# Optimization experiments

Hardware: AMD Instinct MI355X
Metric: run time of the kernel (lower is better)

## Reference

```python
import jax, jax.numpy as jnp
import numpy as np


def setup_inputs() -> dict:
    B, Lq, Lk, D, F, H = 2, 2048, 2048, 128, 128, 8
    key = jax.random.key(0)
    ks = jax.random.split(key, 8)
    X_Q = jax.random.normal(ks[0], (B, Lq, D), dtype=jnp.float32)
    X_K = jax.random.normal(ks[1], (B, Lk, D), dtype=jnp.float32)
    X_V = jax.random.normal(ks[2], (B, Lk, F), dtype=jnp.float32)
    mask = jax.random.randint(ks[3], (B, 1, Lq, Lk), 0, 2, dtype=jnp.int32)
    # xavier_normal for [H, D, D]: std = sqrt(2/(D+D))
    W_Q = jax.random.normal(ks[4], (H, D, D), dtype=jnp.float32) * np.sqrt(2.0 / (D + D))
    W_K = jax.random.normal(ks[5], (H, D, D), dtype=jnp.float32) * np.sqrt(2.0 / (D + D))
    W_V = jax.random.normal(ks[6], (H, F, F), dtype=jnp.float32) * np.sqrt(2.0 / (F + F))
    O = jax.random.normal(ks[7], (F * H, F), dtype=jnp.float32) * np.sqrt(2.0 / (F * H + F))
    return {"X_Q": X_Q, "X_K": X_K, "X_V": X_V, "mask": mask,
            "W_Q": W_Q, "W_K": W_K, "W_V": W_V, "O": O}


def reference(X_Q, X_K, X_V, mask, W_Q, W_K, W_V, O):
    B, Lq, D = X_Q.shape
    H = W_Q.shape[0]
    F = W_V.shape[1]
    # torch.einsum with repeated in-operand index ('hdd') takes the diagonal
    dq = jnp.diagonal(W_Q, axis1=1, axis2=2)  # [H, D]
    dk = jnp.diagonal(W_K, axis1=1, axis2=2)  # [H, D]
    dv = jnp.diagonal(W_V, axis1=1, axis2=2)  # [H, F]
    g = dq * dk                               # fused per-head QK diagonal scale [H, D]
    scale = 1.0 / jnp.sqrt(jnp.asarray(D, dtype=X_Q.dtype))
    scores = jnp.einsum('bqd,hd,bkd->bhqk', X_Q, g, X_K) * scale  # [B,H,Lq,Lk]
    scores = jnp.where(mask == 0, jnp.asarray(-jnp.inf, scores.dtype), scores)
    A = jax.nn.softmax(scores, axis=-1)
    # O_h = A @ (diag(dv_h) scaled V)
    Oh = jnp.einsum('bhqk,hf,bkf->bhqf', A, dv, X_V)  # [B,H,Lq,F]
    Oh = Oh.transpose(0, 2, 1, 3).reshape(B, Lq, H * F)
    return jnp.einsum('bqx,xf->bqf', Oh, O)
```

## Files before the change

kernel.cpp:

```cpp
#include <hip/hip_runtime.h>

typedef __bf16 bf16;
typedef __bf16 bf16x4 __attribute__((ext_vector_type(4)));
typedef __bf16 bf16x8 __attribute__((ext_vector_type(8)));
typedef float f32x4 __attribute__((ext_vector_type(4)));
typedef unsigned int u32;
typedef unsigned long long u64;

#define B_ 2
#define H_ 8
#define L_ 2048
#define D_ 128
#define F_ 128
#define QT 64
#define KT 64
#define NKT (L_ / KT)

#define WS_KB 0u
#define WS_VT (1u << 20)
#define WS_MB (2u << 20)

#define SMEM_BYTES 75776
#define SP_OFF 65536
#define SP_STRIDE 72
#define LWS_OFF 74752
#define SOH_STRIDE 136
#define SO2_STRIDE 136

__device__ __forceinline__ void dma16(const void* g, void* l) {
    __builtin_amdgcn_global_load_lds(
        (const __attribute__((address_space(1))) u32*)g,
        (__attribute__((address_space(3))) u32*)l, 16, 0, 0);
}

__global__ __launch_bounds__(256)
void prep_all(const float* __restrict__ XK, const float* __restrict__ XV,
              const int* __restrict__ mask, bf16* __restrict__ Kb,
              bf16* __restrict__ Vtb, u64* __restrict__ bits)
{
    const int bid = blockIdx.x;
    const int tid = threadIdx.x;
    if (bid < 8192) {
        int wv = bid * 4 + (tid >> 6);
        int lane = tid & 63;
        size_t base = (size_t)wv * 256;
        #pragma unroll
        for (int s = 0; s < 4; ++s) {
            int m = mask[base + s * 64 + lane];
            u64 bal = __ballot(m != 0);
            if (lane == 0) bits[(size_t)wv * 4 + s] = bal;
        }
    } else if (bid < 8448) {
        int gid = (bid - 8192) * 256 + tid;
        int row = gid >> 4;
        int j   = gid & 15;
        const float* src = XK + (size_t)row * 128 + j * 8;
        float4 v0 = *(const float4*)src;
        float4 v1 = *(const float4*)(src + 4);
        bf16x8 w;
        w[0] = (bf16)v0.x; w[1] = (bf16)v0.y; w[2] = (bf16)v0.z; w[3] = (bf16)v0.w;
        w[4] = (bf16)v1.x; w[5] = (bf16)v1.y; w[6] = (bf16)v1.z; w[7] = (bf16)v1.w;
        int jp = j ^ (row & 15);
        *(bf16x8*)(Kb + (size_t)row * 128 + jp * 8) = w;
    } else {
        int idx  = bid - 8448;
        int tile = idx >> 2;
        int fq   = idx & 3;
        int f    = fq * 32 + (tid & 31);
        int j    = tid >> 5;
        int bb   = tile >> 5, kt = tile & 31;
        const float* src = XV + ((size_t)(bb * L_ + kt * 64 + j * 8)) * F_ + f;
        bf16x8 w;
        #pragma unroll
        for (int jj = 0; jj < 8; ++jj) w[jj] = (bf16)src[(size_t)jj * F_];
        *(bf16x8*)(Vtb + (size_t)tile * 8192 + f * 64 + ((j ^ (f & 7)) * 8)) = w;
    }
}

__global__ __launch_bounds__(256, 2)
void attn_fused_kernel(const float* __restrict__ XQ, const bf16* __restrict__ Kb,
                       const bf16* __restrict__ Vtb, const u64* __restrict__ bits,
                       const float* __restrict__ WQ, const float* __restrict__ WK,
                       const float* __restrict__ WV, const float* __restrict__ Om,
                       float* __restrict__ out)
{
    __shared__ __align__(16) char smem[SMEM_BYTES];
    __shared__ __align__(16) float g_s[128];

    bf16* sK0 = (bf16*)smem;
    bf16* sK1 = (bf16*)(smem + 16384);
    bf16* sV0 = (bf16*)(smem + 32768);
    bf16* sV1 = (bf16*)(smem + 49152);
    bf16* sP  = (bf16*)(smem + SP_OFF);
    float* lws = (float*)(smem + LWS_OFF);
    bf16* sOh  = (bf16*)smem;
    bf16* sO2t = (bf16*)(smem + 17408);

    const int tid  = threadIdx.x;
    const int wave = tid >> 6;
    const int lane = tid & 63;
    const int c    = lane & 15;
    const int quad = lane >> 4;
    const int qt = blockIdx.x, h = blockIdx.y, b = blockIdx.z;
    const int q0 = qt * QT;
    const int mh = wave >> 1;
    const int fh = wave & 1;
    const int fv  = tid & 127;
    const int grp = tid >> 7;

    if (tid < 128) {
        float wq = WQ[(h * D_ + tid) * D_ + tid];
        float wk = WK[(h * D_ + tid) * D_ + tid];
        g_s[tid] = wq * wk * 0.08838834764831845f;
    }
    __syncthreads();

    const char* gKbase = (const char*)Kb + (size_t)(b * L_) * 256;
    const char* gVbase = (const char*)Vtb + (size_t)(b * NKT) * 16384;

    #pragma unroll
    for (int i = 0; i < 4; ++i) dma16(gKbase + i * 4096 + tid * 16, (char*)sK0 + i * 4096 + tid * 16);
    #pragma unroll
    for (int i = 0; i < 4; ++i) dma16(gVbase + i * 4096 + tid * 16, (char*)sV0 + i * 4096 + tid * 16);

    bf16x8 qfrag[4][4];
    #pragma unroll
    for (int mt = 0; mt < 4; ++mt) {
        const float* qrow = XQ + (size_t)(b * L_ + q0 + mt * 16 + c) * D_;
        #pragma unroll
        for (int kc = 0; kc < 4; ++kc) {
            int d0 = kc * 32 + quad * 8;
            float4 v0 = *(const float4*)(qrow + d0);
            float4 v1 = *(const float4*)(qrow + d0 + 4);
            float4 g0 = *(const float4*)(g_s + d0);
            float4 g1 = *(const float4*)(g_s + d0 + 4);
            bf16x8 w;
            w[0] = (bf16)(v0.x * g0.x); w[1] = (bf16)(v0.y * g0.y);
            w[2] = (bf16)(v0.z * g0.z); w[3] = (bf16)(v0.w * g0.w);
            w[4] = (bf16)(v1.x * g1.x); w[5] = (bf16)(v1.y * g1.y);
            w[6] = (bf16)(v1.z * g1.z); w[7] = (bf16)(v1.w * g1.w);
            qfrag[mt][kc] = w;
        }
    }

    f32x4 oacc[2][4];
    #pragma unroll
    for (int mi = 0; mi < 2; ++mi)
        #pragma unroll
        for (int fi = 0; fi < 4; ++fi)
            #pragma unroll
            for (int r = 0; r < 4; ++r) oacc[mi][fi][r] = 0.f;
    float lsum[4] = {0.f, 0.f, 0.f, 0.f};

    const int shift = wave * 16 + quad * 4;

    #pragma unroll 2
    for (int kt = 0; kt < NKT; ++kt) {
        bf16* sK  = (kt & 1) ? sK1 : sK0;
        bf16* sV  = (kt & 1) ? sV1 : sV0;
        bf16* sKn = (kt & 1) ? sK0 : sK1;
        bf16* sVn = (kt & 1) ? sV0 : sV1;

        asm volatile("s_barrier" ::: "memory");

        u64 mb[4];
        #pragma unroll
        for (int mt = 0; mt < 4; ++mt)
            mb[mt] = bits[(size_t)(b * L_ + q0 + mt * 16 + c) * NKT + kt];

        if (kt + 1 < NKT) {
            const char* gk = gKbase + (size_t)(kt + 1) * 16384;
            const char* gv = gVbase + (size_t)(kt + 1) * 16384;
            #pragma unroll
            for (int i = 0; i < 4; ++i) dma16(gk + i * 4096 + tid * 16, (char*)sKn + i * 4096 + tid * 16);
            #pragma unroll
            for (int i = 0; i < 4; ++i) dma16(gv + i * 4096 + tid * 16, (char*)sVn + i * 4096 + tid * 16);
            asm volatile("s_waitcnt vmcnt(12)" ::: "memory");
        } else {
            asm volatile("s_waitcnt vmcnt(4)" ::: "memory");
        }
        asm volatile("s_barrier" ::: "memory");

        f32x4 tacc[4];
        #pragma unroll
        for (int mt = 0; mt < 4; ++mt)
            #pragma unroll
            for (int r = 0; r < 4; ++r) tacc[mt][r] = 0.f;

        const bf16* krow = sK + (wave * 16 + c) * 128;
        #pragma unroll
        for (int kc = 0; kc < 4; ++kc) {
            bf16x8 kfrag = *(const bf16x8*)(krow + (((kc * 4 + quad) ^ c) * 8));
            #pragma unroll
            for (int mt = 0; mt < 4; ++mt)
                tacc[mt] = __builtin_amdgcn_mfma_f32_16x16x32_bf16(kfrag, qfrag[mt][kc], tacc[mt], 0, 0, 0);
        }

        #pragma unroll
        for (int mt = 0; mt < 4; ++mt) {
            bf16x4 pw;
            #pragma unroll
            for (int r = 0; r < 4; ++r) {
                float p = ((mb[mt] >> (shift + r)) & 1ull) ? __expf(tacc[mt][r]) : 0.f;
                lsum[mt] += p;
                pw[r] = (bf16)p;
            }
            *(bf16x4*)(sP + (mt * 16 + c) * SP_STRIDE + shift) = pw;
        }
        asm volatile("s_waitcnt lgkmcnt(0)" ::: "memory");
        asm volatile("s_barrier" ::: "memory");

        #pragma unroll
        for (int kc = 0; kc < 2; ++kc) {
            bf16x8 pfrag[2];
            #pragma unroll
            for (int mi = 0; mi < 2; ++mi)
                pfrag[mi] = *(const bf16x8*)(sP + ((2 * mh + mi) * 16 + c) * SP_STRIDE + kc * 32 + quad * 8);
            #pragma unroll
            for (int fi = 0; fi < 4; ++fi) {
                const bf16* vrow = sV + ((fh * 4 + fi) * 16 + c) * 64;
                bf16x8 vfrag = *(const bf16x8*)(vrow + (((kc * 4 + quad) ^ (c & 7)) * 8));
                #pragma unroll
                for (int mi = 0; mi < 2; ++mi)
                    oacc[mi][fi] = __builtin_amdgcn_mfma_f32_16x16x32_bf16(pfrag[mi], vfrag, oacc[mi][fi], 0, 0, 0);
            }
        }
    }

    #pragma unroll
    for (int mt = 0; mt < 4; ++mt) {
        float v = lsum[mt];
        v += __shfl_xor(v, 16); v += __shfl_xor(v, 32);
        if (lane < 16) lws[wave * 64 + mt * 16 + lane] = v;
    }
    __syncthreads();

    if (tid < 128)
        g_s[tid] = WV[(h * F_ + tid) * F_ + tid];

    float linv[2][4];
    #pragma unroll
    for (int mi = 0; mi < 2; ++mi)
        #pragma unroll
        for (int r = 0; r < 4; ++r) {
            int q_local = (2 * mh + mi) * 16 + quad * 4 + r;
            float s = lws[q_local] + lws[64 + q_local] + lws[128 + q_local] + lws[192 + q_local];
            linv[mi][r] = 1.0f / s;
        }
    #pragma unroll
    for (int mi = 0; mi < 2; ++mi)
        #pragma unroll
        for (int fi = 0; fi < 4; ++fi)
            #pragma unroll
            for (int r = 0; r < 4; ++r) {
                int q_local = (2 * mh + mi) * 16 + quad * 4 + r;
                int f_col   = (fh * 4 + fi) * 16 + c;
                sOh[q_local * SOH_STRIDE + f_col] = (bf16)(oacc[mi][fi][r] * linv[mi][r]);
            }
    __syncthreads();

    #pragma unroll
    for (int i = 0; i < 16; ++i) {
        int fp4 = grp * 64 + i * 4;
        bf16x4 w;
        #pragma unroll
        for (int j = 0; j < 4; ++j) {
            int x = fp4 + j;
            w[j] = (bf16)(Om[(h * F_ + x) * F_ + fv] * g_s[x]);
        }
        *(bf16x4*)(sO2t + fv * SO2_STRIDE + fp4) = w;
    }
    __syncthreads();

    bf16x8 afr[4];
    const bf16* ohrow = sOh + (wave * 16 + c) * SOH_STRIDE;
    #pragma unroll
    for (int kc = 0; kc < 4; ++kc)
        afr[kc] = *(const bf16x8*)(ohrow + kc * 32 + quad * 8);

    #pragma unroll
    for (int nt = 0; nt < 8; ++nt) {
        f32x4 pacc;
        #pragma unroll
        for (int r = 0; r < 4; ++r) pacc[r] = 0.f;
        const bf16* orow = sO2t + (nt * 16 + c) * SO2_STRIDE;
        #pragma unroll
        for (int kc = 0; kc < 4; ++kc) {
            bf16x8 bfrag = *(const bf16x8*)(orow + kc * 32 + quad * 8);
            pacc = __builtin_amdgcn_mfma_f32_16x16x32_bf16(afr[kc], bfrag, pacc, 0, 0, 0);
        }
        #pragma unroll
        for (int r = 0; r < 4; ++r) {
            int qg = q0 + wave * 16 + quad * 4 + r;
            atomicAdd(out + ((size_t)(b * L_ + qg) * F_ + nt * 16 + c), pacc[r]);
        }
    }
}

extern "C" void kernel_launch(void* const* d_in, const int* in_sizes, int n_in,
                              void* d_out, int out_size, void* d_ws, size_t ws_size,
                              hipStream_t stream) {
    const float* XQ   = (const float*)d_in[0];
    const float* XK   = (const float*)d_in[1];
    const float* XV   = (const float*)d_in[2];
    const int*   mask = (const int*)d_in[3];
    const float* WQ   = (const float*)d_in[4];
    const float* WK   = (const float*)d_in[5];
    const float* WV   = (const float*)d_in[6];
    const float* Om   = (const float*)d_in[7];
    float* out = (float*)d_out;

    char* ws = (char*)d_ws;
    bf16* Kb   = (bf16*)(ws + WS_KB);
    bf16* Vtb  = (bf16*)(ws + WS_VT);
    u64*  bits = (u64*)(ws + WS_MB);

    prep_all<<<8704, 256, 0, stream>>>(XK, XV, mask, Kb, Vtb, bits);
    hipMemsetAsync(out, 0, (size_t)out_size * sizeof(float), stream);

    dim3 grid(L_ / QT, H_, B_);
    attn_fused_kernel<<<grid, 256, 0, stream>>>(XQ, Kb, Vtb, bits, WQ, WK, WV, Om, out);
}
```

Baseline: 166.3 us.

## Split attention block work across eight waves instead of four

Raises the fused attention kernel from 256 to 512 threads per block and redistributes the work. Each wave now computes half the query rows for one key slice in QK^T, and one query tile by half the features in PV. The staging copies, softmax sums and output projection are re-partitioned to match. This roughly halves per-wave register state (qfrag, oacc) to allow more resident waves and hide latency. The cost is the same barriers now synchronising twice as many waves, plus more LDS traffic per MFMA because fewer fragments are reused per wave.

```diff
diff --git a/kernel.cpp b/kernel.cpp
--- a/kernel.cpp
+++ b/kernel.cpp
@@ -77,7 +77,7 @@
     }
 }
 
-__global__ __launch_bounds__(256, 2)
+__global__ __launch_bounds__(512, 4)
 void attn_fused_kernel(const float* __restrict__ XQ, const bf16* __restrict__ Kb,
                        const bf16* __restrict__ Vtb, const u64* __restrict__ bits,
                        const float* __restrict__ WQ, const float* __restrict__ WK,
@@ -103,8 +103,11 @@
     const int quad = lane >> 4;
     const int qt = blockIdx.x, h = blockIdx.y, b = blockIdx.z;
     const int q0 = qt * QT;
-    const int mh = wave >> 1;
-    const int fh = wave & 1;
+
+    const int kq   = wave & 3;
+    const int msel = wave >> 2;
+    const int mq = wave & 3;
+    const int fh = wave >> 2;
     const int fv  = tid & 127;
     const int grp = tid >> 7;
 
@@ -119,14 +122,14 @@
     const char* gVbase = (const char*)Vtb + (size_t)(b * NKT) * 16384;
 
     #pragma unroll
-    for (int i = 0; i < 4; ++i) dma16(gKbase + i * 4096 + tid * 16, (char*)sK0 + i * 4096 + tid * 16);
-    #pragma unroll
-    for (int i = 0; i < 4; ++i) dma16(gVbase + i * 4096 + tid * 16, (char*)sV0 + i * 4096 + tid * 16);
-
-    bf16x8 qfrag[4][4];
-    #pragma unroll
-    for (int mt = 0; mt < 4; ++mt) {
-        const float* qrow = XQ + (size_t)(b * L_ + q0 + mt * 16 + c) * D_;
+    for (int i = 0; i < 2; ++i) dma16(gKbase + i * 8192 + tid * 16, (char*)sK0 + i * 8192 + tid * 16);
+    #pragma unroll
+    for (int i = 0; i < 2; ++i) dma16(gVbase + i * 8192 + tid * 16, (char*)sV0 + i * 8192 + tid * 16);
+
+    bf16x8 qfrag[2][4];
+    #pragma unroll
+    for (int mi = 0; mi < 2; ++mi) {
+        const float* qrow = XQ + (size_t)(b * L_ + q0 + (msel * 2 + mi) * 16 + c) * D_;
         #pragma unroll
         for (int kc = 0; kc < 4; ++kc) {
             int d0 = kc * 32 + quad * 8;
@@ -139,20 +142,18 @@
             w[2] = (bf16)(v0.z * g0.z); w[3] = (bf16)(v0.w * g0.w);
             w[4] = (bf16)(v1.x * g1.x); w[5] = (bf16)(v1.y * g1.y);
             w[6] = (bf16)(v1.z * g1.z); w[7] = (bf16)(v1.w * g1.w);
-            qfrag[mt][kc] = w;
-        }
-    }
-
-    f32x4 oacc[2][4];
-    #pragma unroll
-    for (int mi = 0; mi < 2; ++mi)
-        #pragma unroll
-        for (int fi = 0; fi < 4; ++fi)
-            #pragma unroll
-            for (int r = 0; r < 4; ++r) oacc[mi][fi][r] = 0.f;
-    float lsum[4] = {0.f, 0.f, 0.f, 0.f};
-
-    const int shift = wave * 16 + quad * 4;
+            qfrag[mi][kc] = w;
+        }
+    }
+
+    f32x4 oacc[4];
+    #pragma unroll
+    for (int fi = 0; fi < 4; ++fi)
+        #pragma unroll
+        for (int r = 0; r < 4; ++r) oacc[fi][r] = 0.f;
+    float lsum[2] = {0.f, 0.f};
+
+    const int shift = kq * 16 + quad * 4;
 
     #pragma unroll 2
     for (int kt = 0; kt < NKT; ++kt) {
@@ -163,105 +164,99 @@
 
         asm volatile("s_barrier" ::: "memory");
 
-        u64 mb[4];
-        #pragma unroll
-        for (int mt = 0; mt < 4; ++mt)
-            mb[mt] = bits[(size_t)(b * L_ + q0 + mt * 16 + c) * NKT + kt];
+        u64 mb[2];
+        #pragma unroll
+        for (int mi = 0; mi < 2; ++mi)
+            mb[mi] = bits[(size_t)(b * L_ + q0 + (msel * 2 + mi) * 16 + c) * NKT + kt];
 
         if (kt + 1 < NKT) {
             const char* gk = gKbase + (size_t)(kt + 1) * 16384;
             const char* gv = gVbase + (size_t)(kt + 1) * 16384;
             #pragma unroll
-            for (int i = 0; i < 4; ++i) dma16(gk + i * 4096 + tid * 16, (char*)sKn + i * 4096 + tid * 16);
-            #pragma unroll
-            for (int i = 0; i < 4; ++i) dma16(gv + i * 4096 + tid * 16, (char*)sVn + i * 4096 + tid * 16);
-            asm volatile("s_waitcnt vmcnt(12)" ::: "memory");
+            for (int i = 0; i < 2; ++i) dma16(gk + i * 8192 + tid * 16, (char*)sKn + i * 8192 + tid * 16);
+            #pragma unroll
+            for (int i = 0; i < 2; ++i) dma16(gv + i * 8192 + tid * 16, (char*)sVn + i * 8192 + tid * 16);
+            asm volatile("s_waitcnt vmcnt(6)" ::: "memory");
         } else {
-            asm volatile("s_waitcnt vmcnt(4)" ::: "memory");
+            asm volatile("s_waitcnt vmcnt(2)" ::: "memory");
         }
         asm volatile("s_barrier" ::: "memory");
 
-        f32x4 tacc[4];
-        #pragma unroll
-        for (int mt = 0; mt < 4; ++mt)
-            #pragma unroll
-            for (int r = 0; r < 4; ++r) tacc[mt][r] = 0.f;
-
-        const bf16* krow = sK + (wave * 16 + c) * 128;
+        f32x4 tacc[2];
+        #pragma unroll
+        for (int mi = 0; mi < 2; ++mi)
+            #pragma unroll
+            for (int r = 0; r < 4; ++r) tacc[mi][r] = 0.f;
+
+        const bf16* krow = sK + (kq * 16 + c) * 128;
         #pragma unroll
         for (int kc = 0; kc < 4; ++kc) {
             bf16x8 kfrag = *(const bf16x8*)(krow + (((kc * 4 + quad) ^ c) * 8));
             #pragma unroll
-            for (int mt = 0; mt < 4; ++mt)
-                tacc[mt] = __builtin_amdgcn_mfma_f32_16x16x32_bf16(kfrag, qfrag[mt][kc], tacc[mt], 0, 0, 0);
-        }
-
-        #pragma unroll
-        for (int mt = 0; mt < 4; ++mt) {
+            for (int mi = 0; mi < 2; ++mi)
+                tacc[mi] = __builtin_amdgcn_mfma_f32_16x16x32_bf16(kfrag, qfrag[mi][kc], tacc[mi], 0, 0, 0);
+        }
+
+        #pragma unroll
+        for (int mi = 0; mi < 2; ++mi) {
             bf16x4 pw;
             #pragma unroll
             for (int r = 0; r < 4; ++r) {
-                float p = ((mb[mt] >> (shift + r)) & 1ull) ? __expf(tacc[mt][r]) : 0.f;
-                lsum[mt] += p;
+                float p = ((mb[mi] >> (shift + r)) & 1ull) ? __expf(tacc[mi][r]) : 0.f;
+                lsum[mi] += p;
                 pw[r] = (bf16)p;
             }
-            *(bf16x4*)(sP + (mt * 16 + c) * SP_STRIDE + shift) = pw;
+            *(bf16x4*)(sP + ((msel * 2 + mi) * 16 + c) * SP_STRIDE + shift) = pw;
         }
         asm volatile("s_waitcnt lgkmcnt(0)" ::: "memory");
         asm volatile("s_barrier" ::: "memory");
 
         #pragma unroll
         for (int kc = 0; kc < 2; ++kc) {
-            bf16x8 pfrag[2];
-            #pragma unroll
-            for (int mi = 0; mi < 2; ++mi)
-                pfrag[mi] = *(const bf16x8*)(sP + ((2 * mh + mi) * 16 + c) * SP_STRIDE + kc * 32 + quad * 8);
+            bf16x8 pfrag = *(const bf16x8*)(sP + (mq * 16 + c) * SP_STRIDE + kc * 32 + quad * 8);
             #pragma unroll
             for (int fi = 0; fi < 4; ++fi) {
                 const bf16* vrow = sV + ((fh * 4 + fi) * 16 + c) * 64;
                 bf16x8 vfrag = *(const bf16x8*)(vrow + (((kc * 4 + quad) ^ (c & 7)) * 8));
-                #pragma unroll
-                for (int mi = 0; mi < 2; ++mi)
-                    oacc[mi][fi] = __builtin_amdgcn_mfma_f32_16x16x32_bf16(pfrag[mi], vfrag, oacc[mi][fi], 0, 0, 0);
+                oacc[fi] = __builtin_amdgcn_mfma_f32_16x16x32_bf16(pfrag, vfrag, oacc[fi], 0, 0, 0);
             }
         }
     }
 
     #pragma unroll
-    for (int mt = 0; mt < 4; ++mt) {
-        float v = lsum[mt];
+    for (int mi = 0; mi < 2; ++mi) {
+        float v = lsum[mi];
         v += __shfl_xor(v, 16); v += __shfl_xor(v, 32);
-        if (lane < 16) lws[wave * 64 + mt * 16 + lane] = v;
+        if (lane < 16) lws[wave * 32 + mi * 16 + lane] = v;
     }
     __syncthreads();
 
     if (tid < 128)
         g_s[tid] = WV[(h * F_ + tid) * F_ + tid];
 
-    float linv[2][4];
-    #pragma unroll
-    for (int mi = 0; mi < 2; ++mi)
+    float linv[4];
+    #pragma unroll
+    for (int r = 0; r < 4; ++r) {
+        int cc = quad * 4 + r;
+        int base = (mq >> 1) * 4;
+        int off  = (mq & 1) * 16 + cc;
+        float s = lws[(base + 0) * 32 + off] + lws[(base + 1) * 32 + off]
+                + lws[(base + 2) * 32 + off] + lws[(base + 3) * 32 + off];
+        linv[r] = 1.0f / s;
+    }
+    #pragma unroll
+    for (int fi = 0; fi < 4; ++fi)
         #pragma unroll
         for (int r = 0; r < 4; ++r) {
-            int q_local = (2 * mh + mi) * 16 + quad * 4 + r;
-            float s = lws[q_local] + lws[64 + q_local] + lws[128 + q_local] + lws[192 + q_local];
-            linv[mi][r] = 1.0f / s;
-        }
-    #pragma unroll
-    for (int mi = 0; mi < 2; ++mi)
-        #pragma unroll
-        for (int fi = 0; fi < 4; ++fi)
-            #pragma unroll
-            for (int r = 0; r < 4; ++r) {
-                int q_local = (2 * mh + mi) * 16 + quad * 4 + r;
-                int f_col   = (fh * 4 + fi) * 16 + c;
-                sOh[q_local * SOH_STRIDE + f_col] = (bf16)(oacc[mi][fi][r] * linv[mi][r]);
-            }
+            int q_local = mq * 16 + quad * 4 + r;
+            int f_col   = (fh * 4 + fi) * 16 + c;
+            sOh[q_local * SOH_STRIDE + f_col] = (bf16)(oacc[fi][r] * linv[r]);
+        }
     __syncthreads();
 
     #pragma unroll
-    for (int i = 0; i < 16; ++i) {
-        int fp4 = grp * 64 + i * 4;
+    for (int i = 0; i < 8; ++i) {
+        int fp4 = grp * 32 + i * 4;
         bf16x4 w;
         #pragma unroll
         for (int j = 0; j < 4; ++j) {
@@ -272,18 +267,20 @@
     }
     __syncthreads();
 
+    const int pm = wave & 3;
+    const int pf = wave >> 2;
     bf16x8 afr[4];
-    const bf16* ohrow = sOh + (wave * 16 + c) * SOH_STRIDE;
+    const bf16* ohrow = sOh + (pm * 16 + c) * SOH_STRIDE;
     #pragma unroll
     for (int kc = 0; kc < 4; ++kc)
         afr[kc] = *(const bf16x8*)(ohrow + kc * 32 + quad * 8);
 
     #pragma unroll
-    for (int nt = 0; nt < 8; ++nt) {
+    for (int nt = 0; nt < 4; ++nt) {
         f32x4 pacc;
         #pragma unroll
         for (int r = 0; r < 4; ++r) pacc[r] = 0.f;
-        const bf16* orow = sO2t + (nt * 16 + c) * SO2_STRIDE;
+        const bf16* orow = sO2t + ((pf * 4 + nt) * 16 + c) * SO2_STRIDE;
         #pragma unroll
         for (int kc = 0; kc < 4; ++kc) {
             bf16x8 bfrag = *(const bf16x8*)(orow + kc * 32 + quad * 8);
@@ -291,8 +288,8 @@
         }
         #pragma unroll
         for (int r = 0; r < 4; ++r) {
-            int qg = q0 + wave * 16 + quad * 4 + r;
-            atomicAdd(out + ((size_t)(b * L_ + qg) * F_ + nt * 16 + c), pacc[r]);
+            int qg = q0 + pm * 16 + quad * 4 + r;
+            atomicAdd(out + ((size_t)(b * L_ + qg) * F_ + (pf * 4 + nt) * 16 + c), pacc[r]);
         }
     }
 }
@@ -319,5 +316,5 @@
     hipMemsetAsync(out, 0, (size_t)out_size * sizeof(float), stream);
 
     dim3 grid(L_ / QT, H_, B_);
-    attn_fused_kernel<<<grid, 256, 0, stream>>>(XQ, Kb, Vtb, bits, WQ, WK, WV, Om, out);
+    attn_fused_kernel<<<grid, 512, 0, stream>>>(XQ, Kb, Vtb, bits, WQ, WK, WV, Om, out);
 }
```

After: 165.5 us. Within noise of the previous version (-0.5%).
